# Performance work log

Hardware: AMD Instinct MI355X
Metric: run time of the kernel (lower is better)

## Reference

```python
import jax, jax.numpy as jnp
import numpy as np

# dMoE (dropless MoE) single-device forward_once path:
# router -> top-k -> sort tokens by expert -> grouped GEMM (sdd/dsd equivalent) -> weighted scatter-combine.
B, S, H, I, E, K = 4, 2048, 2048, 4096, 8, 2  # batch, seq, hidden, intermediate/expert, n_experts, top_k


def setup_inputs() -> dict:
    key = jax.random.key(0)
    k1, k2, k3, k4 = jax.random.split(key, 4)
    x = jax.random.normal(k1, (B, S, H), jnp.float32)
    router_w = jax.random.normal(k2, (E, H), jnp.float32) * 0.02   # LearnedRouter Linear weight
    w1 = jax.random.normal(k3, (E, H, I), jnp.float32) * 0.02      # SparseMLP w1 (per-expert [H, I])
    w2 = jax.random.normal(k4, (E, I, H), jnp.float32) * 0.02      # SparseMLP w2 (per-expert [I, H])
    return {"x": x, "router_w": router_w, "w1": w1, "w2": w2}


def reference(x, router_w, w1, w2):
    Bv, Sv, Hv = x.shape
    Ev = router_w.shape[0]
    xt = x.reshape(-1, Hv)                                   # [T, H], T = B*S

    # LearnedRouter: logits -> fp32 softmax -> top-k weights/indices
    logits = xt @ router_w.T                                 # [T, E]
    scores = jax.nn.softmax(logits.astype(jnp.float32), axis=-1)
    expert_weights, expert_indices = jax.lax.top_k(scores, K)  # [T, K]

    # indices_and_bins: stable sort of flattened assignments + histogram
    flat_experts = expert_indices.reshape(-1)                # [T*K]
    order = jnp.argsort(flat_experts)                        # stable radix-sort equivalent
    tok = order // K                                         # source token of each dispatched row (ops.gather)
    tokens_per_expert = jnp.bincount(flat_experts, length=Ev).astype(jnp.int32)

    # gather token copies into expert-sorted order
    xs = xt[tok]                                             # [T*K, H]

    # SparseMLP: block-sparse sdd (x @ W1) -> gelu(tanh) -> dsd (@ W2), as grouped GEMMs
    h = jax.lax.ragged_dot(xs, w1, tokens_per_expert)        # [T*K, I]
    h = jax.nn.gelu(h, approximate=True)                     # F.gelu(approximate='tanh')
    out = jax.lax.ragged_dot(h, w2, tokens_per_expert)       # [T*K, H]

    # padded_scatter: weighted combine of top-k expert outputs back to token order
    w_sorted = expert_weights.reshape(-1)[order].astype(out.dtype)  # [T*K]
    y = jnp.zeros_like(xt).at[tok].add(out * w_sorted[:, None])
    return y.reshape(Bv, Sv, Hv), tokens_per_expert
```

## Files before the change

### kernel.cpp

```cpp
#include <hip/hip_runtime.h>
#include <cstdint>
#include <cmath>

#define T_TOK 8192
#define H_DIM 2048
#define I_DIM 4096
#define E_NUM 8
#define NROWS 16384

typedef __bf16 bf16x8 __attribute__((ext_vector_type(8)));
typedef float f32x4 __attribute__((ext_vector_type(4)));

__device__ __forceinline__ uint16_t f2bf(float f) {
  union { float f; uint32_t u; } v; v.f = f;
  uint32_t u = v.u;
  uint32_t r = (u + 0x7fffu + ((u >> 16) & 1u)) >> 16;
  return (uint16_t)r;
}
__device__ __forceinline__ float bf2f(uint32_t b) {
  union { uint32_t u; float f; } v; v.u = b << 16;
  return v.f;
}

__device__ __forceinline__ float gelu_tanh(float x) {
  float u = 0.7978845608028654f * (x + 0.044715f * x * x * x);
  return 0.5f * x * (1.0f + tanhf(u));
}

__global__ __launch_bounds__(256) void router_kernel(
    const float* __restrict__ x, const float* __restrict__ rw,
    int* __restrict__ expert_idx, float* __restrict__ expert_w,
    int* __restrict__ counts) {
  int t = blockIdx.x * 4 + (threadIdx.x >> 6);
  int lane = threadIdx.x & 63;
  const float* xr = x + (size_t)t * H_DIM;
  float acc[E_NUM];
#pragma unroll
  for (int e = 0; e < E_NUM; ++e) acc[e] = 0.f;
  for (int j = 0; j < H_DIM / 64; ++j) {
    float xv = xr[lane + 64 * j];
#pragma unroll
    for (int e = 0; e < E_NUM; ++e) acc[e] += xv * rw[e * H_DIM + lane + 64 * j];
  }
#pragma unroll
  for (int e = 0; e < E_NUM; ++e) {
#pragma unroll
    for (int off = 32; off > 0; off >>= 1) acc[e] += __shfl_xor(acc[e], off);
  }
  if (lane == 0) {
    float mx = acc[0];
#pragma unroll
    for (int e = 1; e < E_NUM; ++e) mx = fmaxf(mx, acc[e]);
    float s[E_NUM]; float sum = 0.f;
#pragma unroll
    for (int e = 0; e < E_NUM; ++e) { s[e] = __expf(acc[e] - mx); sum += s[e]; }
    float inv = 1.f / sum;
#pragma unroll
    for (int e = 0; e < E_NUM; ++e) s[e] *= inv;
    int i0 = 0; float w0 = s[0];
#pragma unroll
    for (int e = 1; e < E_NUM; ++e) if (s[e] > w0) { w0 = s[e]; i0 = e; }
    s[i0] = -1.f;
    int i1 = 0; float w1 = s[0];
#pragma unroll
    for (int e = 1; e < E_NUM; ++e) if (s[e] > w1) { w1 = s[e]; i1 = e; }
    expert_idx[2 * t] = i0; expert_idx[2 * t + 1] = i1;
    expert_w[2 * t] = w0;  expert_w[2 * t + 1] = w1;
    atomicAdd(&counts[i0], 1);
    atomicAdd(&counts[i1], 1);
  }
}

__global__ void plan_kernel(const int* __restrict__ counts, int* __restrict__ offsets,
                            int* __restrict__ tile_meta, int* __restrict__ ntilesp,
                            float* __restrict__ out_counts) {
  if (threadIdx.x == 0 && blockIdx.x == 0) {
    int off = 0, nt = 0;
    for (int e = 0; e < E_NUM; ++e) {
      int cnt = counts[e];
      offsets[e] = off;
      out_counts[e] = (float)cnt;
      int ntile = (cnt + 127) >> 7;
      for (int i = 0; i < ntile; ++i) {
        tile_meta[nt * 4 + 0] = off + i * 128;
        tile_meta[nt * 4 + 1] = (cnt - i * 128) < 128 ? (cnt - i * 128) : 128;
        tile_meta[nt * 4 + 2] = e;
        ++nt;
      }
      off += cnt;
    }
    *ntilesp = nt;
  }
}

__global__ __launch_bounds__(256) void assign_kernel(
    const int* __restrict__ expert_idx, const int* __restrict__ offsets,
    int* __restrict__ cursor, int* __restrict__ row_token, int* __restrict__ slot_of) {
  int i = blockIdx.x * 256 + threadIdx.x;
  int e = expert_idx[i];
  int pos = atomicAdd(&cursor[e], 1);
  int slot = offsets[e] + pos;
  row_token[slot] = i >> 1;
  slot_of[i] = slot;
}

__global__ __launch_bounds__(256) void gather_kernel(
    const float* __restrict__ x, const int* __restrict__ row_token,
    uint16_t* __restrict__ xs) {
  int row = blockIdx.x;
  int tok = row_token[row];
  int c = threadIdx.x * 8;
  const float4* p = (const float4*)(x + (size_t)tok * H_DIM + c);
  float4 v0 = p[0], v1 = p[1];
  uint32_t p0 = (uint32_t)f2bf(v0.x) | ((uint32_t)f2bf(v0.y) << 16);
  uint32_t p1 = (uint32_t)f2bf(v0.z) | ((uint32_t)f2bf(v0.w) << 16);
  uint32_t p2 = (uint32_t)f2bf(v1.x) | ((uint32_t)f2bf(v1.y) << 16);
  uint32_t p3 = (uint32_t)f2bf(v1.z) | ((uint32_t)f2bf(v1.w) << 16);
  uint4 o; o.x = p0; o.y = p1; o.z = p2; o.w = p3;
  *(uint4*)(xs + (size_t)row * H_DIM + c) = o;
}

__global__ __launch_bounds__(256) void transpose_cast(
    const float* __restrict__ in, uint16_t* __restrict__ out, int R, int C) {
  __shared__ float tile[64][33];
  int e = blockIdx.z;
  int c0 = blockIdx.x * 32, r0 = blockIdx.y * 64;
  const float* src = in + (size_t)e * R * C;
  uint16_t* dst = out + (size_t)e * R * C;
  int tx = threadIdx.x, ty = threadIdx.y;
#pragma unroll
  for (int it = 0; it < 8; ++it) {
    int r = ty + it * 8;
    tile[r][tx] = src[(size_t)(r0 + r) * C + c0 + tx];
  }
  __syncthreads();
#pragma unroll
  for (int it = 0; it < 4; ++it) {
    int c = ty + it * 8;
    uint32_t lo = f2bf(tile[2 * tx][c]);
    uint32_t hi = f2bf(tile[2 * tx + 1][c]);
    *(uint32_t*)(dst + (size_t)(c0 + c) * R + r0 + 2 * tx) = lo | (hi << 16);
  }
}

__device__ __forceinline__ void gld16(const uint16_t* g, uint16_t* l) {
  __builtin_amdgcn_global_load_lds(
      (const __attribute__((address_space(1))) uint32_t*)(g),
      (__attribute__((address_space(3))) uint32_t*)(l), 16, 0, 0);
}

template <int N, int K, int KITERS, bool GELU>
__global__ __launch_bounds__(256) void gemm_kernel(
    const uint16_t* __restrict__ A, const uint16_t* __restrict__ Bt,
    uint16_t* __restrict__ C,
    const int* __restrict__ tile_meta, const int* __restrict__ ntilesp) {
  int slot = blockIdx.y;
  if (slot >= *ntilesp) return;
  int row_start = tile_meta[slot * 4 + 0];
  int rows = tile_meta[slot * 4 + 1];
  int e = tile_meta[slot * 4 + 2];
  int n0 = blockIdx.x * 128;

  __shared__ uint16_t As[128 * 32];
  __shared__ uint16_t Bs[128 * 32];

  int tid = threadIdx.x;
  int lane = tid & 63;
  int wave = tid >> 6;
  int wm = (wave & 1) * 64;
  int wn = (wave >> 1) * 64;
  int lm = lane & 15;
  int lq = lane >> 4;

  f32x4 acc[4][4];
#pragma unroll
  for (int i = 0; i < 4; ++i)
#pragma unroll
    for (int j = 0; j < 4; ++j) acc[i][j] = (f32x4){0.f, 0.f, 0.f, 0.f};

  int c0i = tid, c1i = tid + 256;
  int rowA0 = c0i >> 2, segP0 = c0i & 3;
  int rowA1 = c1i >> 2, segP1 = c1i & 3;
  int segL0 = segP0 ^ ((rowA0 >> 1) & 3);
  int segL1 = segP1 ^ ((rowA1 >> 1) & 3);
  int ra0 = rowA0 < rows ? rowA0 : rows - 1;
  int ra1 = rowA1 < rows ? rowA1 : rows - 1;
  const uint16_t* gA0 = A + (size_t)(row_start + ra0) * K + segL0 * 8;
  const uint16_t* gA1 = A + (size_t)(row_start + ra1) * K + segL1 * 8;
  const uint16_t* gB0 = Bt + ((size_t)e * N + n0 + rowA0) * K + segL0 * 8;
  const uint16_t* gB1 = Bt + ((size_t)e * N + n0 + rowA1) * K + segL1 * 8;
  uint16_t* lA0 = As + c0i * 8;
  uint16_t* lA1 = As + c1i * 8;
  uint16_t* lB0 = Bs + c0i * 8;
  uint16_t* lB1 = Bs + c1i * 8;

  for (int kk = 0; kk < KITERS; ++kk) {
    gld16(gA0, lA0);
    gld16(gB0, lB0);
    gld16(gA1, lA1);
    gld16(gB1, lB1);
    gA0 += 32; gA1 += 32; gB0 += 32; gB1 += 32;
    __syncthreads();
    bf16x8 af[4], bfr[4];
#pragma unroll
    for (int mi = 0; mi < 4; ++mi) {
      int r = wm + mi * 16 + lm;
      af[mi] = *(const bf16x8*)(As + r * 32 + (lq ^ ((r >> 1) & 3)) * 8);
    }
#pragma unroll
    for (int ni = 0; ni < 4; ++ni) {
      int r = wn + ni * 16 + lm;
      bfr[ni] = *(const bf16x8*)(Bs + r * 32 + (lq ^ ((r >> 1) & 3)) * 8);
    }
#pragma unroll
    for (int mi = 0; mi < 4; ++mi)
#pragma unroll
      for (int ni = 0; ni < 4; ++ni)
        acc[mi][ni] = __builtin_amdgcn_mfma_f32_16x16x32_bf16(af[mi], bfr[ni], acc[mi][ni], 0, 0, 0);
    __syncthreads();
  }

#pragma unroll
  for (int mi = 0; mi < 4; ++mi) {
#pragma unroll
    for (int r = 0; r < 4; ++r) {
      int lrow = wm + mi * 16 + lq * 4 + r;
      if (lrow < rows) {
        size_t base = (size_t)(row_start + lrow) * N + n0 + wn;
#pragma unroll
        for (int ni = 0; ni < 4; ++ni) {
          float v = acc[mi][ni][r];
          if (GELU) v = gelu_tanh(v);
          C[base + ni * 16 + lm] = f2bf(v);
        }
      }
    }
  }
}

__global__ __launch_bounds__(256) void combine_kernel(
    const uint16_t* __restrict__ outb, const int* __restrict__ slot_of,
    const float* __restrict__ ew, float* __restrict__ y) {
  int t = blockIdx.x;
  int s0 = slot_of[2 * t], s1 = slot_of[2 * t + 1];
  float w0 = ew[2 * t], w1 = ew[2 * t + 1];
  int c = threadIdx.x * 8;
  uint4 a = *(const uint4*)(outb + (size_t)s0 * H_DIM + c);
  uint4 b = *(const uint4*)(outb + (size_t)s1 * H_DIM + c);
  float* yp = y + (size_t)t * H_DIM + c;
  float4 r0, r1;
  r0.x = w0 * bf2f(a.x & 0xffffu) + w1 * bf2f(b.x & 0xffffu);
  r0.y = w0 * bf2f(a.x >> 16)     + w1 * bf2f(b.x >> 16);
  r0.z = w0 * bf2f(a.y & 0xffffu) + w1 * bf2f(b.y & 0xffffu);
  r0.w = w0 * bf2f(a.y >> 16)     + w1 * bf2f(b.y >> 16);
  r1.x = w0 * bf2f(a.z & 0xffffu) + w1 * bf2f(b.z & 0xffffu);
  r1.y = w0 * bf2f(a.z >> 16)     + w1 * bf2f(b.z >> 16);
  r1.z = w0 * bf2f(a.w & 0xffffu) + w1 * bf2f(b.w & 0xffffu);
  r1.w = w0 * bf2f(a.w >> 16)     + w1 * bf2f(b.w >> 16);
  *(float4*)yp = r0;
  *(float4*)(yp + 4) = r1;
}

extern "C" void kernel_launch(void* const* d_in, const int* in_sizes, int n_in,
                              void* d_out, int out_size, void* d_ws, size_t ws_size,
                              hipStream_t stream) {
  const float* x  = (const float*)d_in[0];
  const float* rw = (const float*)d_in[1];
  const float* w1 = (const float*)d_in[2];
  const float* w2 = (const float*)d_in[3];
  float* y = (float*)d_out;
  float* out_counts = y + (size_t)T_TOK * H_DIM;

  char* ws = (char*)d_ws;
  int* counts     = (int*)(ws + 0);
  int* cursor     = (int*)(ws + 64);
  int* ntilesp    = (int*)(ws + 128);
  int* offsets    = (int*)(ws + 192);
  int* tile_meta  = (int*)(ws + 1024);
  int* expert_idx = (int*)(ws + 8192);
  float* expert_w = (float*)(ws + 8192 + 65536);
  int* row_token  = (int*)(ws + 8192 + 2 * 65536);
  int* slot_of    = (int*)(ws + 8192 + 3 * 65536);
  const size_t MB = 1ull << 20;
  uint16_t* xs   = (uint16_t*)(ws + 1 * MB);
  uint16_t* hbuf = (uint16_t*)(ws + 66 * MB);
  uint16_t* outb = (uint16_t*)(ws + 194 * MB);
  uint16_t* w1t  = (uint16_t*)(ws + 258 * MB);
  uint16_t* w2t  = (uint16_t*)(ws + 386 * MB);

  hipMemsetAsync(d_ws, 0, 8192, stream);

  router_kernel<<<T_TOK / 4, 256, 0, stream>>>(x, rw, expert_idx, expert_w, counts);
  plan_kernel<<<1, 64, 0, stream>>>(counts, offsets, tile_meta, ntilesp, out_counts);
  assign_kernel<<<NROWS / 256, 256, 0, stream>>>(expert_idx, offsets, cursor, row_token, slot_of);
  gather_kernel<<<NROWS, 256, 0, stream>>>(x, row_token, xs);
  transpose_cast<<<dim3(I_DIM / 32, H_DIM / 64, E_NUM), dim3(32, 8), 0, stream>>>(w1, w1t, H_DIM, I_DIM);
  transpose_cast<<<dim3(H_DIM / 32, I_DIM / 64, E_NUM), dim3(32, 8), 0, stream>>>(w2, w2t, I_DIM, H_DIM);
  gemm_kernel<I_DIM, H_DIM, H_DIM / 32, true>
      <<<dim3(I_DIM / 128, 144), 256, 0, stream>>>(xs, w1t, hbuf, tile_meta, ntilesp);
  gemm_kernel<H_DIM, I_DIM, I_DIM / 32, false>
      <<<dim3(H_DIM / 128, 144), 256, 0, stream>>>(hbuf, w2t, outb, tile_meta, ntilesp);
  combine_kernel<<<T_TOK, 256, 0, stream>>>(outb, slot_of, expert_w, y);
}
```

Baseline: 1.626 ms.

## Use 256x256 tiles with double-buffered async LDS pipeline in grouped GEMMs

```diff
diff --git a/kernel.cpp b/kernel.cpp
--- a/kernel.cpp
+++ b/kernel.cpp
@@ -80,10 +80,11 @@
       int cnt = counts[e];
       offsets[e] = off;
       out_counts[e] = (float)cnt;
-      int ntile = (cnt + 127) >> 7;
+      int ntile = (cnt + 255) >> 8;
       for (int i = 0; i < ntile; ++i) {
-        tile_meta[nt * 4 + 0] = off + i * 128;
-        tile_meta[nt * 4 + 1] = (cnt - i * 128) < 128 ? (cnt - i * 128) : 128;
+        int rem = cnt - i * 256;
+        tile_meta[nt * 4 + 0] = off + i * 256;
+        tile_meta[nt * 4 + 1] = rem < 256 ? rem : 256;
         tile_meta[nt * 4 + 2] = e;
         ++nt;
       }
@@ -149,8 +150,8 @@
       (__attribute__((address_space(3))) uint32_t*)(l), 16, 0, 0);
 }
 
-template <int N, int K, int KITERS, bool GELU>
-__global__ __launch_bounds__(256) void gemm_kernel(
+template <int N, int K, bool GELU>
+__global__ __launch_bounds__(512, 2) void gemm256(
     const uint16_t* __restrict__ A, const uint16_t* __restrict__ Bt,
     uint16_t* __restrict__ C,
     const int* __restrict__ tile_meta, const int* __restrict__ ntilesp) {
@@ -159,74 +160,117 @@
   int row_start = tile_meta[slot * 4 + 0];
   int rows = tile_meta[slot * 4 + 1];
   int e = tile_meta[slot * 4 + 2];
-  int n0 = blockIdx.x * 128;
-
-  __shared__ uint16_t As[128 * 32];
-  __shared__ uint16_t Bs[128 * 32];
+  int n0 = blockIdx.x * 256;
+  constexpr int KT = K / 64;
+
+  extern __shared__ uint16_t smem[];
 
   int tid = threadIdx.x;
   int lane = tid & 63;
   int wave = tid >> 6;
-  int wm = (wave & 1) * 64;
-  int wn = (wave >> 1) * 64;
+  int wr = wave >> 2;
+  int wc = wave & 3;
   int lm = lane & 15;
   int lq = lane >> 4;
 
-  f32x4 acc[4][4];
-#pragma unroll
-  for (int i = 0; i < 4; ++i)
+  f32x4 acc[8][4];
+#pragma unroll
+  for (int i = 0; i < 8; ++i)
 #pragma unroll
     for (int j = 0; j < 4; ++j) acc[i][j] = (f32x4){0.f, 0.f, 0.f, 0.f};
 
-  int c0i = tid, c1i = tid + 256;
-  int rowA0 = c0i >> 2, segP0 = c0i & 3;
-  int rowA1 = c1i >> 2, segP1 = c1i & 3;
-  int segL0 = segP0 ^ ((rowA0 >> 1) & 3);
-  int segL1 = segP1 ^ ((rowA1 >> 1) & 3);
-  int ra0 = rowA0 < rows ? rowA0 : rows - 1;
-  int ra1 = rowA1 < rows ? rowA1 : rows - 1;
-  const uint16_t* gA0 = A + (size_t)(row_start + ra0) * K + segL0 * 8;
-  const uint16_t* gA1 = A + (size_t)(row_start + ra1) * K + segL1 * 8;
-  const uint16_t* gB0 = Bt + ((size_t)e * N + n0 + rowA0) * K + segL0 * 8;
-  const uint16_t* gB1 = Bt + ((size_t)e * N + n0 + rowA1) * K + segL1 * 8;
-  uint16_t* lA0 = As + c0i * 8;
-  uint16_t* lA1 = As + c1i * 8;
-  uint16_t* lB0 = Bs + c0i * 8;
-  uint16_t* lB1 = Bs + c1i * 8;
-
-  for (int kk = 0; kk < KITERS; ++kk) {
-    gld16(gA0, lA0);
-    gld16(gB0, lB0);
-    gld16(gA1, lA1);
-    gld16(gB1, lB1);
-    gA0 += 32; gA1 += 32; gB0 += 32; gB1 += 32;
-    __syncthreads();
-    bf16x8 af[4], bfr[4];
-#pragma unroll
-    for (int mi = 0; mi < 4; ++mi) {
-      int r = wm + mi * 16 + lm;
-      af[mi] = *(const bf16x8*)(As + r * 32 + (lq ^ ((r >> 1) & 3)) * 8);
+  int r0c = tid >> 2, sP0 = tid & 3;
+  int r1c = r0c + 128;
+  int sL0 = sP0 ^ ((r0c >> 1) & 3);
+  int rac0 = r0c < rows ? r0c : rows - 1;
+  int rac1 = r1c < rows ? r1c : rows - 1;
+  const uint16_t* gA0 = A + (size_t)(row_start + rac0) * K + sL0 * 8;
+  const uint16_t* gA1 = A + (size_t)(row_start + rac1) * K + sL0 * 8;
+  const uint16_t* gB0 = Bt + ((size_t)e * N + n0 + r0c) * K + sL0 * 8;
+  const uint16_t* gB1 = Bt + ((size_t)e * N + n0 + r1c) * K + sL0 * 8;
+
+  auto stageA = [&](uint16_t* dst, int koff) {
+    gld16(gA0 + koff, dst + tid * 8);
+    gld16(gA1 + koff, dst + (tid + 512) * 8);
+  };
+  auto stageB = [&](uint16_t* dst, int koff) {
+    gld16(gB0 + koff, dst + tid * 8);
+    gld16(gB1 + koff, dst + (tid + 512) * 8);
+  };
+
+  stageA(smem + 0, 0);        stageB(smem + 16384, 0);
+  stageA(smem + 8192, 32);    stageB(smem + 24576, 32);
+  stageA(smem + 32768, 64);   stageB(smem + 49152, 64);
+  asm volatile("s_waitcnt vmcnt(8)" ::: "memory");
+  __builtin_amdgcn_s_barrier();
+
+  bf16x8 af[8], bfr[4];
+  for (int t = 0; t < KT; ++t) {
+    int s = t & 1;
+    uint16_t* Ls = smem + s * 32768;
+    uint16_t* Lo = smem + (s ^ 1) * 32768;
+    int kt1 = (t + 1 < KT) ? t + 1 : KT - 1;
+    int kt2 = (t + 2 < KT) ? t + 2 : KT - 1;
+
+#pragma unroll
+    for (int mi = 0; mi < 8; ++mi) {
+      int r = wr * 128 + mi * 16 + lm;
+      af[mi] = *(const bf16x8*)(Ls + r * 32 + (lq ^ ((r >> 1) & 3)) * 8);
     }
 #pragma unroll
     for (int ni = 0; ni < 4; ++ni) {
-      int r = wn + ni * 16 + lm;
-      bfr[ni] = *(const bf16x8*)(Bs + r * 32 + (lq ^ ((r >> 1) & 3)) * 8);
-    }
-#pragma unroll
-    for (int mi = 0; mi < 4; ++mi)
+      int r = wc * 64 + ni * 16 + lm;
+      bfr[ni] = *(const bf16x8*)(Ls + 16384 + r * 32 + (lq ^ ((r >> 1) & 3)) * 8);
+    }
+    stageA(Lo + 8192, kt1 * 64 + 32);
+    stageB(Lo + 24576, kt1 * 64 + 32);
+    asm volatile("s_waitcnt vmcnt(8)" ::: "memory");
+    __builtin_amdgcn_s_barrier();
+    asm volatile("s_waitcnt lgkmcnt(0)" ::: "memory");
+    __builtin_amdgcn_sched_barrier(0);
+    __builtin_amdgcn_s_setprio(1);
+#pragma unroll
+    for (int mi = 0; mi < 8; ++mi)
 #pragma unroll
       for (int ni = 0; ni < 4; ++ni)
         acc[mi][ni] = __builtin_amdgcn_mfma_f32_16x16x32_bf16(af[mi], bfr[ni], acc[mi][ni], 0, 0, 0);
-    __syncthreads();
-  }
-
-#pragma unroll
-  for (int mi = 0; mi < 4; ++mi) {
+    __builtin_amdgcn_s_setprio(0);
+    __builtin_amdgcn_s_barrier();
+
+#pragma unroll
+    for (int mi = 0; mi < 8; ++mi) {
+      int r = wr * 128 + mi * 16 + lm;
+      af[mi] = *(const bf16x8*)(Ls + 8192 + r * 32 + (lq ^ ((r >> 1) & 3)) * 8);
+    }
+#pragma unroll
+    for (int ni = 0; ni < 4; ++ni) {
+      int r = wc * 64 + ni * 16 + lm;
+      bfr[ni] = *(const bf16x8*)(Ls + 24576 + r * 32 + (lq ^ ((r >> 1) & 3)) * 8);
+    }
+    stageA(Ls, kt2 * 64);
+    stageB(Ls + 16384, kt2 * 64);
+    asm volatile("s_waitcnt vmcnt(8)" ::: "memory");
+    __builtin_amdgcn_s_barrier();
+    asm volatile("s_waitcnt lgkmcnt(0)" ::: "memory");
+    __builtin_amdgcn_sched_barrier(0);
+    __builtin_amdgcn_s_setprio(1);
+#pragma unroll
+    for (int mi = 0; mi < 8; ++mi)
+#pragma unroll
+      for (int ni = 0; ni < 4; ++ni)
+        acc[mi][ni] = __builtin_amdgcn_mfma_f32_16x16x32_bf16(af[mi], bfr[ni], acc[mi][ni], 0, 0, 0);
+    __builtin_amdgcn_s_setprio(0);
+    __builtin_amdgcn_s_barrier();
+  }
+  asm volatile("s_waitcnt vmcnt(0)" ::: "memory");
+
+#pragma unroll
+  for (int mi = 0; mi < 8; ++mi) {
+    int lrow = wr * 128 + mi * 16 + lq * 4;
 #pragma unroll
     for (int r = 0; r < 4; ++r) {
-      int lrow = wm + mi * 16 + lq * 4 + r;
-      if (lrow < rows) {
-        size_t base = (size_t)(row_start + lrow) * N + n0 + wn;
+      if (lrow + r < rows) {
+        size_t base = (size_t)(row_start + lrow + r) * N + n0 + wc * 64;
 #pragma unroll
         for (int ni = 0; ni < 4; ++ni) {
           float v = acc[mi][ni][r];
@@ -288,6 +332,15 @@
   uint16_t* w1t  = (uint16_t*)(ws + 258 * MB);
   uint16_t* w2t  = (uint16_t*)(ws + 386 * MB);
 
+  static bool attr_set = false;
+  if (!attr_set) {
+    attr_set = true;
+    hipFuncSetAttribute(reinterpret_cast<const void*>(&gemm256<I_DIM, H_DIM, true>),
+                        hipFuncAttributeMaxDynamicSharedMemorySize, 131072);
+    hipFuncSetAttribute(reinterpret_cast<const void*>(&gemm256<H_DIM, I_DIM, false>),
+                        hipFuncAttributeMaxDynamicSharedMemorySize, 131072);
+  }
+
   hipMemsetAsync(d_ws, 0, 8192, stream);
 
   router_kernel<<<T_TOK / 4, 256, 0, stream>>>(x, rw, expert_idx, expert_w, counts);
@@ -296,9 +349,9 @@
   gather_kernel<<<NROWS, 256, 0, stream>>>(x, row_token, xs);
   transpose_cast<<<dim3(I_DIM / 32, H_DIM / 64, E_NUM), dim3(32, 8), 0, stream>>>(w1, w1t, H_DIM, I_DIM);
   transpose_cast<<<dim3(H_DIM / 32, I_DIM / 64, E_NUM), dim3(32, 8), 0, stream>>>(w2, w2t, I_DIM, H_DIM);
-  gemm_kernel<I_DIM, H_DIM, H_DIM / 32, true>
-      <<<dim3(I_DIM / 128, 144), 256, 0, stream>>>(xs, w1t, hbuf, tile_meta, ntilesp);
-  gemm_kernel<H_DIM, I_DIM, I_DIM / 32, false>
-      <<<dim3(H_DIM / 128, 144), 256, 0, stream>>>(hbuf, w2t, outb, tile_meta, ntilesp);
+  gemm256<I_DIM, H_DIM, true>
+      <<<dim3(I_DIM / 256, 72), 512, 131072, stream>>>(xs, w1t, hbuf, tile_meta, ntilesp);
+  gemm256<H_DIM, I_DIM, false>
+      <<<dim3(H_DIM / 256, 72), 512, 131072, stream>>>(hbuf, w2t, outb, tile_meta, ntilesp);
   combine_kernel<<<T_TOK, 256, 0, stream>>>(outb, slot_of, expert_w, y);
 }
```

New measurement: 1.638 ms. About the same (+0.7%).
